# Optimization experiments

Measured on AMD Instinct MI355X. Metric: run time of the kernel, lower is better.

## Reference

```python
import jax, jax.numpy as jnp
import numpy as np

ALPHA = 1.702  # GLU sigmoid scale
LIMIT = 7.0    # clamp limit
B, S, H, E, F, TOP_K = 2, 1024, 768, 16, 768, 4


def setup_inputs() -> dict:
    key = jax.random.key(0)
    ks = jax.random.split(key, 7)
    return {
        "hidden_states": jax.random.normal(ks[0], (B, S, H), jnp.float32),
        "router_weight": jax.random.normal(ks[1], (E, H), jnp.float32) * 0.02,
        "router_bias": jax.random.normal(ks[2], (E,), jnp.float32) * 0.02,
        "gate_up_proj": jax.random.normal(ks[3], (E, H, 2 * F), jnp.float32) * 0.02,
        "gate_up_proj_bias": jax.random.normal(ks[4], (E, 2 * F), jnp.float32) * 0.02,
        "down_proj": jax.random.normal(ks[5], (E, F, H), jnp.float32) * 0.02,
        "down_proj_bias": jax.random.normal(ks[6], (E, H), jnp.float32) * 0.02,
        "top_k": TOP_K,
    }


def reference(hidden_states, router_weight, router_bias, gate_up_proj,
              gate_up_proj_bias, down_proj, down_proj_bias, top_k):
    b, s, h = hidden_states.shape
    x = hidden_states.reshape(-1, h)                      # [T, H]
    t = x.shape[0]
    # ---- TopK router ----
    logits = x @ router_weight.T + router_bias            # [T, E]
    top_val, top_idx = jax.lax.top_k(logits, top_k)       # [T, K]
    top_val = jax.nn.softmax(top_val, axis=-1)
    router_scores = jnp.zeros_like(logits).at[
        jnp.arange(t)[:, None], top_idx].set(top_val)     # [T, E]
    # ---- Dense (all-expert) FFN, as in the reference repeat+bmm ----
    gate_up = jnp.einsum('th,ehf->etf', x, gate_up_proj) \
        + gate_up_proj_bias[:, None, :]                   # [E, T, 2F]
    gate = jnp.minimum(gate_up[..., 0::2], LIMIT)         # clamp(max=limit)
    up = jnp.clip(gate_up[..., 1::2], -LIMIT, LIMIT)
    glu = gate * jax.nn.sigmoid(gate * ALPHA)
    expert_out = jnp.einsum('etf,efh->eth', (up + 1.0) * glu, down_proj) \
        + down_proj_bias[:, None, :]                      # [E, T, H]
    expert_out = expert_out.reshape(-1, b, s, h)          # [E, B, S, H]
    w = router_scores.T.reshape(-1, b, s)[..., None]      # [E, B, S, 1]
    routed_out = (expert_out * w).sum(axis=0)             # [B, S, H]
    return routed_out, router_scores
```

## Files before the change

kernel.cpp:

```cpp
#include <hip/hip_runtime.h>
#include <hip/hip_bf16.h>

#define T_TOK 2048
#define H_DIM 768
#define E_NUM 16
#define F_DIM 768
#define TWOF 1536
#define TOPK 4
#define NASSIGN 8192
#define BM 128
#define BK 64
#define KT 12
#define NTILE 80
#define NSLOTP (NTILE * BM)
#define MAXT1 10
#define CHUNK (BM * BK)
#define WTILE (64 * BK)
#define NRTR 256

typedef __bf16 bf16x8 __attribute__((ext_vector_type(8)));
typedef unsigned short us8 __attribute__((ext_vector_type(8)));
typedef float f32x4 __attribute__((ext_vector_type(4)));

__device__ __forceinline__ unsigned short f2bf(float f) {
  unsigned u = __float_as_uint(f);
  u += 0x7FFF + ((u >> 16) & 1);
  return (unsigned short)(u >> 16);
}

__device__ __forceinline__ void gl_lds16(const unsigned short* g, unsigned short* l) {
  __builtin_amdgcn_global_load_lds(
      (const __attribute__((address_space(1))) unsigned int*)g,
      (__attribute__((address_space(3))) unsigned int*)l, 16, 0, 0);
}

__global__ __launch_bounds__(256)
void router_kernel(const float* __restrict__ x, const float* __restrict__ rw,
                   const float* __restrict__ rb, float* __restrict__ scores,
                   int* __restrict__ tk_idx, float* __restrict__ tk_w,
                   int* __restrict__ tmap, float* __restrict__ wgrp,
                   unsigned short* __restrict__ xg) {
  __shared__ float lg[8][16], sc[8][16];
  const int bid = blockIdx.x;
  const int tid = threadIdx.x;
  const int t0 = bid * 8;
  if (tid < 40) {
    tmap[bid * 40 + tid] = 0;
    wgrp[bid * 40 + tid] = 0.0f;
  }
  {
    const int tokr = tid >> 5;
    const int g0 = tid & 31;
    const float* xs = x + (size_t)(t0 + tokr) * H_DIM;
    unsigned short* xd = xg + (size_t)(t0 + tokr) * H_DIM;
    #pragma unroll
    for (int i = 0; i < 3; ++i) {
      const int gg = g0 + i * 32;
      const f32x4 a = *(const f32x4*)(xs + gg * 8);
      const f32x4 b = *(const f32x4*)(xs + gg * 8 + 4);
      us8 o;
      #pragma unroll
      for (int j = 0; j < 4; ++j) { o[j] = f2bf(a[j]); o[4 + j] = f2bf(b[j]); }
      *(us8*)&xd[gg * 8] = o;
    }
  }
  const int lane32 = tid & 31, tok = tid >> 5;
  const int e = lane32 & 15, q2 = lane32 >> 4;
  const int t = t0 + tok;
  const float* xr = x + (size_t)t * H_DIM + q2 * 384;
  const float* wr = rw + (size_t)e * H_DIM + q2 * 384;
  double a0 = 0, a1 = 0, a2 = 0, a3 = 0;
  #pragma unroll 4
  for (int h = 0; h < 384; h += 4) {
    const f32x4 xv = *(const f32x4*)(xr + h);
    const f32x4 wv = *(const f32x4*)(wr + h);
    a0 += (double)xv[0] * (double)wv[0];
    a1 += (double)xv[1] * (double)wv[1];
    a2 += (double)xv[2] * (double)wv[2];
    a3 += (double)xv[3] * (double)wv[3];
  }
  double acc = (a0 + a1) + (a2 + a3);
  acc += __shfl_xor(acc, 16, 64);
  if (q2 == 0) lg[tok][e] = (float)acc + rb[e];
  __syncthreads();
  if (lane32 == 0) {
    float v[16];
    #pragma unroll
    for (int i = 0; i < 16; ++i) { v[i] = lg[tok][i]; sc[tok][i] = 0.0f; }
    int idx[TOPK]; float val[TOPK];
    for (int k = 0; k < TOPK; ++k) {
      float best = -3.4e38f; int bi = 0;
      for (int i = 0; i < 16; ++i)
        if (v[i] > best) { best = v[i]; bi = i; }
      idx[k] = bi; val[k] = best; v[bi] = -3.4e38f;
    }
    float s = 0.0f, ev[TOPK];
    for (int k = 0; k < TOPK; ++k) { ev[k] = expf(val[k] - val[0]); s += ev[k]; }
    for (int k = 0; k < TOPK; ++k) {
      float wgt = ev[k] / s;
      sc[tok][idx[k]] = wgt;
      tk_idx[t * TOPK + k] = idx[k];
      tk_w[t * TOPK + k] = wgt;
    }
  }
  __syncthreads();
  if (tid < 128)
    scores[(size_t)(t0 + (tid >> 4)) * 16 + (tid & 15)] = sc[tid >> 4][tid & 15];
}

__global__ __launch_bounds__(512)
void convert_w_kernel(const float* __restrict__ gup, const float* __restrict__ dwn,
                      unsigned short* __restrict__ gw, unsigned short* __restrict__ uw,
                      unsigned short* __restrict__ dw,
                      const int* __restrict__ tk_idx, const float* __restrict__ tk_w,
                      int* __restrict__ counts, int* __restrict__ offs,
                      int* __restrict__ tmap, float* __restrict__ wgrp) {
  const int ft = blockIdx.x, kt = blockIdx.y, z = blockIdx.z;
  const int tid = threadIdx.x;
  const int n = tid & 63, k8 = tid >> 6;
  const int doff = n * BK + 8 * (k8 ^ (n & 7));
  __shared__ unsigned short tg[WTILE], tu[WTILE];
  if (z < 16) {
    const int e = z;
    const float* src = gup + ((size_t)(e * H_DIM + kt * 64 + k8 * 8)) * TWOF
                           + 2 * (ft * 64 + n);
    us8 g, u;
    #pragma unroll
    for (int j = 0; j < 8; ++j) {
      const float2 p = *(const float2*)(src + (size_t)j * TWOF);
      g[j] = f2bf(p.x); u[j] = f2bf(p.y);
    }
    *(us8*)&tg[doff] = g;
    *(us8*)&tu[doff] = u;
    __syncthreads();
    const size_t tb = (((size_t)e * KT + kt) * 12 + ft) * WTILE;
    *(us8*)&gw[tb + tid * 8] = *(const us8*)&tg[tid * 8];
    *(us8*)&uw[tb + tid * 8] = *(const us8*)&tu[tid * 8];
  } else {
    const int e = z - 16;
    const float* src = dwn + ((size_t)(e * F_DIM + kt * 64 + k8 * 8)) * H_DIM
                           + ft * 64 + n;
    us8 o;
    #pragma unroll
    for (int j = 0; j < 8; ++j) o[j] = f2bf(src[(size_t)j * H_DIM]);
    *(us8*)&tg[doff] = o;
    __syncthreads();
    const size_t tb = (((size_t)e * KT + kt) * 12 + ft) * WTILE;
    *(us8*)&dw[tb + tid * 8] = *(const us8*)&tg[tid * 8];
  }
  if (ft == 0 && kt == 0 && z == 0) {
    __shared__ int hist[256][16];
    __shared__ int seg[16][16];
    __shared__ int cnt[16], eoff[16];
    int loc[16];
    int eid[32];
    if (tid < 256) {
      #pragma unroll
      for (int e = 0; e < 16; ++e) loc[e] = 0;
      const int base = tid * 32;
      for (int i = 0; i < 32; ++i) { int e = tk_idx[base + i]; eid[i] = e; loc[e]++; }
      #pragma unroll
      for (int e = 0; e < 16; ++e) hist[tid][e] = loc[e];
    }
    __syncthreads();
    const int s = (tid >> 4) & 15, e16 = tid & 15;
    if (tid < 256) {
      int sum = 0;
      #pragma unroll
      for (int j = 0; j < 16; ++j) sum += hist[s * 16 + j][e16];
      seg[s][e16] = sum;
    }
    __syncthreads();
    if (tid < 16) {
      int run = 0;
      #pragma unroll
      for (int s2 = 0; s2 < 16; ++s2) { int t = seg[s2][tid]; seg[s2][tid] = run; run += t; }
      cnt[tid] = run;
    }
    __syncthreads();
    if (tid < 256) {
      int run = seg[s][e16];
      #pragma unroll
      for (int j = 0; j < 16; ++j) { int t = hist[s * 16 + j][e16]; hist[s * 16 + j][e16] = run; run += t; }
    }
    __syncthreads();
    if (tid == 0) {
      int acc = 0;
      for (int e = 0; e < 16; ++e) { eoff[e] = acc; acc += (cnt[e] + BM - 1) / BM * BM; }
    }
    __syncthreads();
    if (tid < 16) { counts[tid] = cnt[tid]; offs[tid] = eoff[tid]; }
    if (tid < 256) {
      int run[16];
      #pragma unroll
      for (int e = 0; e < 16; ++e) run[e] = hist[tid][e];
      const int base = tid * 32;
      for (int i = 0; i < 32; ++i) {
        int e = eid[i];
        int slot = eoff[e] + run[e]++;
        tmap[slot] = base + i;
        wgrp[slot] = tk_w[base + i];
      }
    }
  }
}

__global__ __launch_bounds__(512)
void gemm1_kernel(const unsigned short* __restrict__ xg, const unsigned short* __restrict__ gw,
                  const unsigned short* __restrict__ uw, const float* __restrict__ gupb,
                  const int* __restrict__ counts, const int* __restrict__ offs,
                  const int* __restrict__ tmap, unsigned short* __restrict__ act) {
  const int bid = blockIdx.x;
  const int swz = (bid & 7) * 120 + (bid >> 3);
  const int ey = swz / 6, ft = swz % 6;
  const int e = ey / MAXT1, tile = ey % MAXT1;
  const int count = counts[e];
  if (tile * BM >= count) return;
  const int tileg = (offs[e] >> 7) + tile;
  const int tid = threadIdx.x;
  const int wv = tid >> 6, lane = tid & 63;
  const int ml = lane & 15, lh = lane >> 4;
  const int wm = wv >> 2, wn = wv & 3;

  __shared__ unsigned short lA[CHUNK];
  __shared__ unsigned short lBg[CHUNK];
  __shared__ unsigned short lBu[CHUNK];

  const int arow = tid >> 3;
  const int agr = (tid & 7) ^ (arow & 7);
  const int t0 = tmap[tileg * BM + arow] >> 2;
  const int t1 = tmap[tileg * BM + 64 + arow] >> 2;
  const unsigned short* a0 = xg + (size_t)t0 * H_DIM + agr * 8;
  const unsigned short* a1 = xg + (size_t)t1 * H_DIM + agr * 8;

  const unsigned short* gb = gw + ((size_t)e * KT * 12 + ft * 2) * WTILE;
  const unsigned short* ub = uw + ((size_t)e * KT * 12 + ft * 2) * WTILE;

  f32x4 accg[4][2] = {};
  f32x4 accu[4][2] = {};

  for (int kt = 0; kt < KT; ++kt) {
    const unsigned short* gs = gb + (size_t)kt * 12 * WTILE;
    const unsigned short* us = ub + (size_t)kt * 12 * WTILE;
    gl_lds16(a0 + kt * 64, &lA[tid * 8]);
    gl_lds16(a1 + kt * 64, &lA[(512 + tid) * 8]);
    gl_lds16(gs + tid * 8, &lBg[tid * 8]);
    gl_lds16(gs + (512 + tid) * 8, &lBg[(512 + tid) * 8]);
    gl_lds16(us + tid * 8, &lBu[tid * 8]);
    gl_lds16(us + (512 + tid) * 8, &lBu[(512 + tid) * 8]);
    __syncthreads();
    #pragma unroll
    for (int ks = 0; ks < 2; ++ks) {
      const int slot = ks * 4 + lh;
      bf16x8 af[4];
      #pragma unroll
      for (int mf = 0; mf < 4; ++mf) {
        const int ar = wm * 64 + mf * 16 + ml;
        af[mf] = __builtin_bit_cast(bf16x8, *(const us8*)&lA[ar * BK + 8 * (slot ^ (ar & 7))]);
      }
      #pragma unroll
      for (int nf = 0; nf < 2; ++nf) {
        const int br = wn * 32 + nf * 16 + ml;
        const int ba = (br >> 6) * WTILE + (br & 63) * BK + 8 * (slot ^ (br & 7));
        bf16x8 bg = __builtin_bit_cast(bf16x8, *(const us8*)&lBg[ba]);
        bf16x8 bu = __builtin_bit_cast(bf16x8, *(const us8*)&lBu[ba]);
        #pragma unroll
        for (int mf = 0; mf < 4; ++mf) {
          accg[mf][nf] = __builtin_amdgcn_mfma_f32_16x16x32_bf16(af[mf], bg, accg[mf][nf], 0, 0, 0);
          accu[mf][nf] = __builtin_amdgcn_mfma_f32_16x16x32_bf16(af[mf], bu, accu[mf][nf], 0, 0, 0);
        }
      }
    }
    __syncthreads();
  }
  unsigned short* tbuf = (wn & 2) ? lBg : lA;
  #pragma unroll
  for (int mf = 0; mf < 4; ++mf) {
    #pragma unroll
    for (int nf = 0; nf < 2; ++nf) {
      const int fcl = wn * 32 + nf * 16 + ml;
      const int c = fcl & 63;
      const int fc = ft * 128 + fcl;
      const float bgv = gupb[(size_t)e * TWOF + 2 * fc];
      const float buv = gupb[(size_t)e * TWOF + 2 * fc + 1];
      #pragma unroll
      for (int r = 0; r < 4; ++r) {
        const int m = wm * 64 + mf * 16 + lh * 4 + r;
        float g = accg[mf][nf][r] + bgv;
        float u = accu[mf][nf][r] + buv;
        g = fminf(g, 7.0f);
        u = fminf(fmaxf(u, -7.0f), 7.0f);
        const float glu = g / (1.0f + __expf(-1.702f * g));
        tbuf[m * BK + 8 * ((c >> 3) ^ (m & 7)) + (c & 7)] = f2bf((u + 1.0f) * glu);
      }
    }
  }
  __syncthreads();
  unsigned short* ob0 = act + ((size_t)tileg * KT + ft * 2) * CHUNK;
  unsigned short* ob1 = ob0 + CHUNK;
  #pragma unroll
  for (int i = 0; i < 2; ++i) {
    *(us8*)&ob0[(i * 512 + tid) * 8] = *(const us8*)&lA[(i * 512 + tid) * 8];
    *(us8*)&ob1[(i * 512 + tid) * 8] = *(const us8*)&lBg[(i * 512 + tid) * 8];
  }
}

__global__ __launch_bounds__(512)
void gemm2_kernel(const unsigned short* __restrict__ act, const unsigned short* __restrict__ dw,
                  const float* __restrict__ dwnb, const int* __restrict__ counts,
                  const int* __restrict__ offs, const int* __restrict__ tmap,
                  const float* __restrict__ wgrp, unsigned short* __restrict__ partial) {
  const int bid = blockIdx.x;
  const int swz = (bid & 7) * 120 + (bid >> 3);
  const int ey = swz / 6, ft = swz % 6;
  const int e = ey / MAXT1, tile = ey % MAXT1;
  const int count = counts[e];
  if (tile * BM >= count) return;
  const int off = offs[e];
  const int tileg = (off >> 7) + tile;
  const int tid = threadIdx.x;
  const int wv = tid >> 6, lane = tid & 63;
  const int ml = lane & 15, lh = lane >> 4;
  const int wm = wv >> 2, wn = wv & 3;

  __shared__ unsigned short lA[CHUNK];
  __shared__ unsigned short lB[CHUNK];

  const unsigned short* ab = act + (size_t)tileg * KT * CHUNK;
  const unsigned short* bb = dw + ((size_t)e * KT * 12 + ft * 2) * WTILE;

  f32x4 acc[4][2] = {};

  for (int kt = 0; kt < KT; ++kt) {
    const unsigned short* as = ab + kt * CHUNK;
    const unsigned short* bs = bb + (size_t)kt * 12 * WTILE;
    gl_lds16(as + tid * 8, &lA[tid * 8]);
    gl_lds16(as + (512 + tid) * 8, &lA[(512 + tid) * 8]);
    gl_lds16(bs + tid * 8, &lB[tid * 8]);
    gl_lds16(bs + (512 + tid) * 8, &lB[(512 + tid) * 8]);
    __syncthreads();
    #pragma unroll
    for (int ks = 0; ks < 2; ++ks) {
      const int slot = ks * 4 + lh;
      bf16x8 af[4];
      #pragma unroll
      for (int mf = 0; mf < 4; ++mf) {
        const int ar = wm * 64 + mf * 16 + ml;
        af[mf] = __builtin_bit_cast(bf16x8, *(const us8*)&lA[ar * BK + 8 * (slot ^ (ar & 7))]);
      }
      #pragma unroll
      for (int nf = 0; nf < 2; ++nf) {
        const int br = wn * 32 + nf * 16 + ml;
        const int ba = (br >> 6) * WTILE + (br & 63) * BK + 8 * (slot ^ (br & 7));
        bf16x8 bv = __builtin_bit_cast(bf16x8, *(const us8*)&lB[ba]);
        #pragma unroll
        for (int mf = 0; mf < 4; ++mf)
          acc[mf][nf] = __builtin_amdgcn_mfma_f32_16x16x32_bf16(af[mf], bv, acc[mf][nf], 0, 0, 0);
      }
    }
    __syncthreads();
  }
  #pragma unroll
  for (int mf = 0; mf < 4; ++mf) {
    #pragma unroll
    for (int nf = 0; nf < 2; ++nf) {
      const int hc = ft * 128 + wn * 32 + nf * 16 + ml;
      const float bias = dwnb[(size_t)e * H_DIM + hc];
      #pragma unroll
      for (int r = 0; r < 4; ++r) {
        const int m = tile * BM + wm * 64 + mf * 16 + lh * 4 + r;
        if (m < count) {
          const int slot = off + m;
          partial[(size_t)tmap[slot] * H_DIM + hc] =
              f2bf(wgrp[slot] * (acc[mf][nf][r] + bias));
        }
      }
    }
  }
}

__global__ __launch_bounds__(256)
void reduce_kernel(const unsigned short* __restrict__ partial, float* __restrict__ out) {
  const int idx = blockIdx.x * 256 + threadIdx.x;
  const int t = idx / 96, g = idx - (idx / 96) * 96;
  const int h0 = g * 8;
  float s[8] = {0, 0, 0, 0, 0, 0, 0, 0};
  #pragma unroll
  for (int k = 0; k < 4; ++k) {
    const us8 p = *(const us8*)&partial[(size_t)(t * 4 + k) * H_DIM + h0];
    #pragma unroll
    for (int j = 0; j < 8; ++j)
      s[j] += __uint_as_float((unsigned)p[j] << 16);
  }
  f32x4 o0 = {s[0], s[1], s[2], s[3]};
  f32x4 o1 = {s[4], s[5], s[6], s[7]};
  *(f32x4*)&out[(size_t)t * H_DIM + h0] = o0;
  *(f32x4*)&out[(size_t)t * H_DIM + h0 + 4] = o1;
}

extern "C" void kernel_launch(void* const* d_in, const int* in_sizes, int n_in,
                              void* d_out, int out_size, void* d_ws, size_t ws_size,
                              hipStream_t stream) {
  const float* x    = (const float*)d_in[0];
  const float* rw   = (const float*)d_in[1];
  const float* rb   = (const float*)d_in[2];
  const float* gup  = (const float*)d_in[3];
  const float* gupb = (const float*)d_in[4];
  const float* dwn  = (const float*)d_in[5];
  const float* dwnb = (const float*)d_in[6];
  float* out = (float*)d_out;
  float* scores = out + (size_t)T_TOK * H_DIM;

  char* w = (char*)d_ws;
  int*   tk_idx = (int*)w;            w += NASSIGN * 4;
  float* tk_w   = (float*)w;          w += NASSIGN * 4;
  int*   counts = (int*)w;            w += 64;
  int*   offs   = (int*)w;            w += 64;
  int*   tmap   = (int*)w;            w += NSLOTP * 4;
  float* wgrp   = (float*)w;          w += NSLOTP * 4;
  unsigned short* gw = (unsigned short*)w; w += (size_t)E_NUM * KT * 12 * WTILE * 2;
  unsigned short* uw = (unsigned short*)w; w += (size_t)E_NUM * KT * 12 * WTILE * 2;
  unsigned short* dw = (unsigned short*)w; w += (size_t)E_NUM * KT * 12 * WTILE * 2;
  unsigned short* xg = (unsigned short*)w; w += (size_t)T_TOK * H_DIM * 2;
  unsigned short* act = (unsigned short*)w; w += (size_t)NTILE * KT * CHUNK * 2;
  unsigned short* partial = (unsigned short*)w; w += (size_t)NASSIGN * H_DIM * 2;

  router_kernel<<<NRTR, 256, 0, stream>>>(x, rw, rb, scores, tk_idx, tk_w, tmap, wgrp, xg);
  convert_w_kernel<<<dim3(12, 12, 32), 512, 0, stream>>>(
      gup, dwn, gw, uw, dw, tk_idx, tk_w, counts, offs, tmap, wgrp);
  gemm1_kernel<<<6 * E_NUM * MAXT1, 512, 0, stream>>>(
      xg, gw, uw, gupb, counts, offs, tmap, act);
  gemm2_kernel<<<6 * E_NUM * MAXT1, 512, 0, stream>>>(
      act, dw, dwnb, counts, offs, tmap, wgrp, partial);
  reduce_kernel<<<(T_TOK * 96) / 256, 256, 0, stream>>>(partial, out);
}
```

Measured before the change: 107.6 us.

## Restructure weight conversion for coalesced reads and k-major swizzled tile layout

The weight-conversion kernel now has each block read 8 full contiguous rows of the fp32 gate/up or down weights with 16-byte vector loads, instead of strided 8-byte/4-byte column reads. The packed bf16 tile layout changes from n-major to k-slot-major with an XOR swizzle on n, and the GEMM B-operand LDS addressing is updated to match. The aim is to cut uncoalesced global traffic in the fp32-to-bf16 conversion, which moves a large volume of weights per call. The cost is a different LDS read pattern in the GEMMs that could bring bank conflicts, and the routing histogram now reuses the shared buffer after an extra sync.

```diff
diff --git a/kernel.cpp b/kernel.cpp
--- a/kernel.cpp
+++ b/kernel.cpp
@@ -115,52 +115,79 @@
                       const int* __restrict__ tk_idx, const float* __restrict__ tk_w,
                       int* __restrict__ counts, int* __restrict__ offs,
                       int* __restrict__ tmap, float* __restrict__ wgrp) {
-  const int ft = blockIdx.x, kt = blockIdx.y, z = blockIdx.z;
+  const int xe = blockIdx.x;
+  const int e = xe / 12, kt = xe % 12;
+  const int r8 = blockIdx.y;
+  const int z = blockIdx.z;
   const int tid = threadIdx.x;
-  const int n = tid & 63, k8 = tid >> 6;
-  const int doff = n * BK + 8 * (k8 ^ (n & 7));
-  __shared__ unsigned short tg[WTILE], tu[WTILE];
-  if (z < 16) {
-    const int e = z;
-    const float* src = gup + ((size_t)(e * H_DIM + kt * 64 + k8 * 8)) * TWOF
-                           + 2 * (ft * 64 + n);
-    us8 g, u;
-    #pragma unroll
-    for (int j = 0; j < 8; ++j) {
-      const float2 p = *(const float2*)(src + (size_t)j * TWOF);
-      g[j] = f2bf(p.x); u[j] = f2bf(p.y);
-    }
-    *(us8*)&tg[doff] = g;
-    *(us8*)&tu[doff] = u;
-    __syncthreads();
-    const size_t tb = (((size_t)e * KT + kt) * 12 + ft) * WTILE;
-    *(us8*)&gw[tb + tid * 8] = *(const us8*)&tg[tid * 8];
-    *(us8*)&uw[tb + tid * 8] = *(const us8*)&tu[tid * 8];
+  __shared__ unsigned short buf[12288];
+  __shared__ int seg[16][16];
+  __shared__ int cnt[16], eoff[16];
+  if (z == 0) {
+    unsigned short* lg = buf;
+    unsigned short* lu = buf + 6144;
+    const float* src = gup + ((size_t)(e * H_DIM + kt * 64 + r8 * 8)) * TWOF;
+    #pragma unroll
+    for (int i = 0; i < 6; ++i) {
+      const int q = i * 512 + tid;
+      const f32x4 v = *(const f32x4*)(src + 4 * q);
+      const int row = q / 384;
+      const int fp = (q - row * 384) * 2;
+      const int a = row * 768 + fp;
+      *(unsigned*)&lg[a] = (unsigned)f2bf(v[0]) | ((unsigned)f2bf(v[2]) << 16);
+      *(unsigned*)&lu[a] = (unsigned)f2bf(v[1]) | ((unsigned)f2bf(v[3]) << 16);
+    }
+    __syncthreads();
+    #pragma unroll
+    for (int i = 0; i < 3; ++i) {
+      const int o = i * 512 + tid;
+      const int which = o / 768;
+      const int rem = o - which * 768;
+      const int ft = rem >> 6, n = rem & 63;
+      const unsigned short* ls = which ? lu : lg;
+      us8 v;
+      #pragma unroll
+      for (int j = 0; j < 8; ++j) v[j] = ls[j * 768 + rem];
+      unsigned short* dst = (which ? uw : gw)
+          + (((size_t)e * KT + kt) * 12 + ft) * WTILE + r8 * 512 + ((n ^ (r8 & 7)) << 3);
+      *(us8*)dst = v;
+    }
   } else {
-    const int e = z - 16;
-    const float* src = dwn + ((size_t)(e * F_DIM + kt * 64 + k8 * 8)) * H_DIM
-                           + ft * 64 + n;
-    us8 o;
-    #pragma unroll
-    for (int j = 0; j < 8; ++j) o[j] = f2bf(src[(size_t)j * H_DIM]);
-    *(us8*)&tg[doff] = o;
-    __syncthreads();
-    const size_t tb = (((size_t)e * KT + kt) * 12 + ft) * WTILE;
-    *(us8*)&dw[tb + tid * 8] = *(const us8*)&tg[tid * 8];
-  }
-  if (ft == 0 && kt == 0 && z == 0) {
-    __shared__ int hist[256][16];
-    __shared__ int seg[16][16];
-    __shared__ int cnt[16], eoff[16];
+    unsigned short* lv = buf;
+    const float* src = dwn + ((size_t)(e * F_DIM + kt * 64 + r8 * 8)) * H_DIM;
+    #pragma unroll
+    for (int i = 0; i < 3; ++i) {
+      const int q = i * 512 + tid;
+      const f32x4 v = *(const f32x4*)(src + 4 * q);
+      const int row = q / 192;
+      const int c = (q - row * 192) * 4;
+      const int a = row * 768 + c;
+      *(unsigned*)&lv[a]     = (unsigned)f2bf(v[0]) | ((unsigned)f2bf(v[1]) << 16);
+      *(unsigned*)&lv[a + 2] = (unsigned)f2bf(v[2]) | ((unsigned)f2bf(v[3]) << 16);
+    }
+    __syncthreads();
+    for (int o = tid; o < 768; o += 512) {
+      const int ft = o >> 6, n = o & 63;
+      us8 v;
+      #pragma unroll
+      for (int j = 0; j < 8; ++j) v[j] = lv[j * 768 + o];
+      unsigned short* dst = dw
+          + (((size_t)e * KT + kt) * 12 + ft) * WTILE + r8 * 512 + ((n ^ (r8 & 7)) << 3);
+      *(us8*)dst = v;
+    }
+  }
+  if (xe == 0 && r8 == 0 && z == 0) {
+    int (*hist)[16] = (int(*)[16])buf;
+    __syncthreads();
     int loc[16];
     int eid[32];
     if (tid < 256) {
       #pragma unroll
-      for (int e = 0; e < 16; ++e) loc[e] = 0;
+      for (int e2 = 0; e2 < 16; ++e2) loc[e2] = 0;
       const int base = tid * 32;
-      for (int i = 0; i < 32; ++i) { int e = tk_idx[base + i]; eid[i] = e; loc[e]++; }
-      #pragma unroll
-      for (int e = 0; e < 16; ++e) hist[tid][e] = loc[e];
+      for (int i = 0; i < 32; ++i) { int e2 = tk_idx[base + i]; eid[i] = e2; loc[e2]++; }
+      #pragma unroll
+      for (int e2 = 0; e2 < 16; ++e2) hist[tid][e2] = loc[e2];
     }
     __syncthreads();
     const int s = (tid >> 4) & 15, e16 = tid & 15;
@@ -186,18 +213,18 @@
     __syncthreads();
     if (tid == 0) {
       int acc = 0;
-      for (int e = 0; e < 16; ++e) { eoff[e] = acc; acc += (cnt[e] + BM - 1) / BM * BM; }
+      for (int e2 = 0; e2 < 16; ++e2) { eoff[e2] = acc; acc += (cnt[e2] + BM - 1) / BM * BM; }
     }
     __syncthreads();
     if (tid < 16) { counts[tid] = cnt[tid]; offs[tid] = eoff[tid]; }
     if (tid < 256) {
       int run[16];
       #pragma unroll
-      for (int e = 0; e < 16; ++e) run[e] = hist[tid][e];
+      for (int e2 = 0; e2 < 16; ++e2) run[e2] = hist[tid][e2];
       const int base = tid * 32;
       for (int i = 0; i < 32; ++i) {
-        int e = eid[i];
-        int slot = eoff[e] + run[e]++;
+        int e2 = eid[i];
+        int slot = eoff[e2] + run[e2]++;
         tmap[slot] = base + i;
         wgrp[slot] = tk_w[base + i];
       }
@@ -261,7 +288,7 @@
       #pragma unroll
       for (int nf = 0; nf < 2; ++nf) {
         const int br = wn * 32 + nf * 16 + ml;
-        const int ba = (br >> 6) * WTILE + (br & 63) * BK + 8 * (slot ^ (br & 7));
+        const int ba = (br >> 6) * WTILE + slot * 512 + (((br & 63) ^ (slot & 7)) << 3);
         bf16x8 bg = __builtin_bit_cast(bf16x8, *(const us8*)&lBg[ba]);
         bf16x8 bu = __builtin_bit_cast(bf16x8, *(const us8*)&lBu[ba]);
         #pragma unroll
@@ -351,7 +378,7 @@
       #pragma unroll
       for (int nf = 0; nf < 2; ++nf) {
         const int br = wn * 32 + nf * 16 + ml;
-        const int ba = (br >> 6) * WTILE + (br & 63) * BK + 8 * (slot ^ (br & 7));
+        const int ba = (br >> 6) * WTILE + slot * 512 + (((br & 63) ^ (slot & 7)) << 3);
         bf16x8 bv = __builtin_bit_cast(bf16x8, *(const us8*)&lB[ba]);
         #pragma unroll
         for (int mf = 0; mf < 4; ++mf)
@@ -426,7 +453,7 @@
   unsigned short* partial = (unsigned short*)w; w += (size_t)NASSIGN * H_DIM * 2;
 
   router_kernel<<<NRTR, 256, 0, stream>>>(x, rw, rb, scores, tk_idx, tk_w, tmap, wgrp, xg);
-  convert_w_kernel<<<dim3(12, 12, 32), 512, 0, stream>>>(
+  convert_w_kernel<<<dim3(192, 8, 2), 512, 0, stream>>>(
       gup, dwn, gw, uw, dw, tk_idx, tk_w, counts, offs, tmap, wgrp);
   gemm1_kernel<<<6 * E_NUM * MAXT1, 512, 0, stream>>>(
       xg, gw, uw, gupb, counts, offs, tmap, act);
```

Result: no change. 106.1 us (-1.4%).
